# Optimization experiments

Hardware: AMD Instinct MI355X
Metric: run time of the kernel (lower is better)

The kernel has to match this reference:

```python
import jax, jax.numpy as jnp
import numpy as np

B, S, D, H = 4, 1024, 1024, 16
E = D // H  # head_dim = 64
N = 2 * H  # number of slots


def _ln(x, g, b, eps=1e-5):
    m = x.mean(-1, keepdims=True)
    v = ((x - m) ** 2).mean(-1, keepdims=True)
    return (x - m) / jnp.sqrt(v + eps) * g + b


def _feat(x):
    # F.elu(x, 1.0) + 1.0
    return jax.nn.elu(x) + 1.0


def setup_inputs() -> dict:
    key = jax.random.key(0)
    ks = jax.random.split(key, 40)
    w = lambda k, shape: jax.random.normal(k, shape, jnp.float32) * 0.02
    z = lambda shape: jnp.zeros(shape, jnp.float32)
    o = lambda shape: jnp.ones(shape, jnp.float32)
    return {
        'x': jax.random.normal(ks[0], (B, S, D), jnp.float32),
        'ln1_g': o(D), 'ln1_b': z(D), 'ln2_g': o(D), 'ln2_b': z(D),
        'Wq': w(ks[1], (D, D)), 'bq': z(D),
        'Wk': w(ks[2], (D, D)), 'bk': z(D),
        'Wv': w(ks[3], (D, D)), 'bv': z(D),
        'Wf': w(ks[4], (D, D)), 'bf': z(D),
        'Wr1': w(ks[5], (D, 2 * D)), 'br1': z(2 * D),
        'Wr2': w(ks[6], (2 * D, D)), 'br2': z(D),
        'Wip': w(ks[7], (D, N * E)), 'bip': z(N * E),
        'Wtq': w(ks[8], (E, E)), 'btq': z(E),
        'Wtk': w(ks[9], (E, E)), 'btk': z(E),
        'Wtv': w(ks[10], (E, E)), 'btv': z(E),
        'lnp_g': o(E), 'lnp_b': z(E),
        'Wl1': w(ks[11], (E, 2 * E)), 'bl1': z(2 * E),
        'Wl2': w(ks[12], (2 * E, E)), 'bl2': z(E),
        'Wsp': w(ks[13], (2 * E, E)), 'bsp': z(E),
    }


def reference(x, ln1_g, ln1_b, ln2_g, ln2_b, Wq, bq, Wk, bk, Wv, bv, Wf, bf,
              Wr1, br1, Wr2, br2, Wip, bip, Wtq, btq, Wtk, btk, Wtv, btv,
              lnp_g, lnp_b, Wl1, bl1, Wl2, bl2, Wsp, bsp):
    xn = _ln(x, ln1_g, ln1_b)
    # main q/k/v
    q = (xn @ Wq + bq).reshape(B, S, H, E).transpose(0, 2, 1, 3) / np.sqrt(E)  # [B,H,S,E]
    k = (xn @ Wk + bk).reshape(B, S, H, E)
    v = (xn @ Wv + bv).reshape(B, S, H, E)
    kv0 = jnp.concatenate([k, v], axis=2)  # [B,S,2H,E] initial slots

    # --- competitive (slot) attention, 3 iterations ---
    inp = (xn @ Wip + bip).reshape(B, S, N, E)
    kk = _feat(inp @ Wtk + btk)          # [B,S,N,E]
    vv = inp @ Wtv + btv                 # [B,S,N,E]
    slots = kv0
    scale = 1.0 / E                      # slot_size = head_dim
    for _ in range(3):
        qq = (slots @ Wtq + btq) + kv0
        qq = _feat(qq * (E ** -0.5))
        logits = jnp.einsum('bswe,bsne->bswn', kk, qq)
        attn = jax.nn.softmax(logits, axis=3) + 1e-6
        attn = attn / attn.sum(axis=2, keepdims=True)
        upd = jnp.einsum('bswn,bswe->bsne', attn, vv)
        h = _ln(upd, lnp_g, lnp_b)
        h = jax.nn.relu(h @ Wl1 + bl1) @ Wl2 + bl2
        slots = slots + h * scale
    # slot_dropout is eval-mode identity
    slots = jnp.concatenate([kv0, slots], axis=-1) @ Wsp + bsp  # [B,S,2H,E]

    k2 = slots[:, :, :H].transpose(0, 2, 3, 1)  # [B,H,E,S]
    v2 = slots[:, :, H:].transpose(0, 2, 1, 3)  # [B,H,S,E]
    qf = _feat(q)
    kf = _feat(k2)
    score = qf @ kf                              # [B,H,S,S]
    score = score / (score.sum(-1, keepdims=True) + 1e-5)
    out = (score @ v2).transpose(0, 2, 1, 3).reshape(B, S, D)
    out = out @ Wf + bf
    out = x + out
    res = out
    h = _ln(out, ln2_g, ln2_b)
    h = jax.nn.relu(h @ Wr1 + br1) @ Wr2 + br2  # dropouts are eval-mode identity
    return res + h
```

## Files before the change

kernel.cpp:

```cpp
#include <hip/hip_runtime.h>
#include <hip/hip_bf16.h>

typedef __hip_bfloat16 bf16t;
typedef short short8 __attribute__((ext_vector_type(8)));
typedef short short4v __attribute__((ext_vector_type(4)));
typedef float f32x4 __attribute__((ext_vector_type(4)));


__device__ __forceinline__ float featf(float x) { return x > 0.f ? x + 1.f : __expf(x); }
__device__ __forceinline__ float featf_s(float x) { return x > 0.f ? x + 1.f : expf(x); }
__device__ __forceinline__ float frcp(float x) { return __builtin_amdgcn_rcpf(x); }
__device__ __forceinline__ float ldf(const bf16t* p, size_t i) { return __bfloat162float(p[i]); }
__device__ __forceinline__ float ldf(const float* p, size_t i) { return p[i]; }
__device__ __forceinline__ void stf(bf16t* p, size_t i, float v) { p[i] = __float2bfloat16(v); }
__device__ __forceinline__ void stf(float* p, size_t i, float v) { p[i] = v; }
__device__ __forceinline__ float b2f(unsigned short u) {
    unsigned int x = ((unsigned int)u) << 16; float f; __builtin_memcpy(&f, &x, 4); return f;
}
__device__ __forceinline__ unsigned short f2b(float f) {
    bf16t h = __float2bfloat16(f); unsigned short u; __builtin_memcpy(&u, &h, 2); return u;
}
__device__ __forceinline__ void gl_lds16(const short* g, short* l) {
    __builtin_amdgcn_global_load_lds((const __attribute__((address_space(1))) unsigned int*)g,
                                     (__attribute__((address_space(3))) unsigned int*)l, 16, 0, 0);
}
#define MFMA16(a, b, c) __builtin_amdgcn_mfma_f32_16x16x32_bf16((a), (b), (c), 0, 0, 0)

__global__ __launch_bounds__(256) void fill_k(float* __restrict__ out, int n, float v) {
    int i = blockIdx.x * 256 + threadIdx.x;
    if (i < n) out[i] = v;
}

__global__ __launch_bounds__(256) void multi_transpose_k(const float* __restrict__ s0, const float* __restrict__ s1,
                                                         const float* __restrict__ s2, const float* __restrict__ s3,
                                                         bf16t* __restrict__ d0, bf16t* __restrict__ d1,
                                                         bf16t* __restrict__ d2, bf16t* __restrict__ d3,
                                                         int R0, int C0, int R1, int C1, int R2, int C2, int R3, int C3,
                                                         int e0, int e1, int e2) {
    __shared__ bf16t tile[32][33];
    int b = blockIdx.x;
    const float* W; bf16t* Wt; int C, R, lb;
    if (b < e0)      { W = s0; Wt = d0; R = R0; C = C0; lb = b; }
    else if (b < e1) { W = s1; Wt = d1; R = R1; C = C1; lb = b - e0; }
    else if (b < e2) { W = s2; Wt = d2; R = R2; C = C2; lb = b - e1; }
    else             { W = s3; Wt = d3; R = R3; C = C3; lb = b - e2; }
    int tiles_c = C >> 5;
    int c0 = (lb % tiles_c) * 32, r0 = (lb / tiles_c) * 32;
    int tx = threadIdx.x & 31, ty = threadIdx.x >> 5;
    #pragma unroll
    for (int i = 0; i < 32; i += 8)
        tile[ty + i][tx] = __float2bfloat16(W[(size_t)(r0 + ty + i) * C + (c0 + tx)]);
    __syncthreads();
    #pragma unroll
    for (int i = 0; i < 32; i += 8)
        Wt[(size_t)(c0 + ty + i) * R + (r0 + tx)] = tile[tx][ty + i];
}

__global__ __launch_bounds__(256) void small_prep_k(const float* __restrict__ Wtk,
                                                    const float* __restrict__ Wtv,
                                                    const float* __restrict__ Wtq,
                                                    const float* __restrict__ Wl1,
                                                    const float* __restrict__ Wl2,
                                                    const float* __restrict__ Wsp,
                                                    const float* __restrict__ bk,
                                                    const float* __restrict__ bv,
                                                    const float* __restrict__ bip,
                                                    const float* __restrict__ bq,
                                                    const float* __restrict__ btk,
                                                    const float* __restrict__ btv,
                                                    bf16t* __restrict__ WtkvT,
                                                    bf16t* __restrict__ WtqI,
                                                    bf16t* __restrict__ Wl1T,
                                                    bf16t* __restrict__ Wl2T,
                                                    bf16t* __restrict__ WspT,
                                                    float* __restrict__ bcat,
                                                    float* __restrict__ bcat2) {
    int b = blockIdx.x, tid = threadIdx.x;
    if (b == 0) {
        for (int i = tid; i < 8192; i += 256) {
            int n2 = i >> 6, e = i & 63;
            float v = (n2 < 64) ? Wtk[e * 64 + n2] : Wtv[e * 64 + (n2 - 64)];
            WtkvT[i] = __float2bfloat16(v);
        }
    } else if (b == 1) {
        for (int i = tid; i < 8192; i += 256) {
            int e = i >> 7, k = i & 127;
            float v = (k < 64) ? Wtq[k * 64 + e] : ((k - 64 == e) ? 1.f : 0.f);
            WtqI[i] = __float2bfloat16(v);
        }
    } else if (b == 2) {
        for (int i = tid; i < 8192; i += 256) { int n = i >> 6, k = i & 63; Wl1T[i] = __float2bfloat16(Wl1[k * 128 + n]); }
    } else if (b == 3) {
        for (int i = tid; i < 8192; i += 256) { int n = i >> 7, k = i & 127; Wl2T[i] = __float2bfloat16(Wl2[k * 64 + n]); }
    } else if (b == 4) {
        for (int i = tid; i < 8192; i += 256) { int n = i >> 7, k = i & 127; WspT[i] = __float2bfloat16(Wsp[k * 64 + n]); }
    } else if (b == 5) {
        for (int i = tid; i < 5120; i += 256) {
            float v;
            if (i < 1024) v = bk[i];
            else if (i < 2048) v = bv[i - 1024];
            else if (i < 4096) v = bip[i - 2048];
            else v = bq[i - 4096];
            bcat[i] = v;
        }
    } else {
        if (tid < 128) bcat2[tid] = (tid < 64) ? btk[tid] : btv[tid - 64];
    }
}

__global__ __launch_bounds__(256) void ln_kernel(const float* __restrict__ X,
                                                 const float* __restrict__ g,
                                                 const float* __restrict__ b,
                                                 bf16t* __restrict__ Y) {
    int t = blockIdx.x, tid = threadIdx.x;
    size_t base = (size_t)t * 1024 + tid * 4;
    float v0 = X[base + 0], v1 = X[base + 1], v2 = X[base + 2], v3 = X[base + 3];
    float s = v0 + v1 + v2 + v3;
    float q = v0 * v0 + v1 * v1 + v2 * v2 + v3 * v3;
    __shared__ float rs[4], rq[4];
    for (int o = 32; o > 0; o >>= 1) { s += __shfl_down(s, o); q += __shfl_down(q, o); }
    int wid = tid >> 6, lane = tid & 63;
    if (lane == 0) { rs[wid] = s; rq[wid] = q; }
    __syncthreads();
    float S = rs[0] + rs[1] + rs[2] + rs[3];
    float Q = rq[0] + rq[1] + rq[2] + rq[3];
    float mean = S * (1.f / 1024.f);
    float var = Q * (1.f / 1024.f) - mean * mean;
    float rstd = rsqrtf(var + 1e-5f);
    int c = tid * 4;
    stf(Y, base + 0, (v0 - mean) * rstd * g[c + 0] + b[c + 0]);
    stf(Y, base + 1, (v1 - mean) * rstd * g[c + 1] + b[c + 1]);
    stf(Y, base + 2, (v2 - mean) * rstd * g[c + 2] + b[c + 2]);
    stf(Y, base + 3, (v3 - mean) * rstd * g[c + 3] + b[c + 3]);
}

template <int MODE, typename TC, typename TADD>
__global__ __launch_bounds__(256) void gemm64_k(const bf16t* __restrict__ A,
                                                const bf16t* __restrict__ Bt,
                                                const float* __restrict__ bias,
                                                const TADD* __restrict__ add,
                                                TC* __restrict__ C,
                                                int M, int N, int K, int ldC) {
    __shared__ short As[64 * 32];
    __shared__ short Bs[128 * 32];
    int tid = threadIdx.x;
    int wave = tid >> 6, lane = tid & 63;
    int l16 = lane & 15, quad = lane >> 4;
    int tilesM = M >> 6;
    int bid = (blockIdx.x & 7) * (gridDim.x >> 3) + (blockIdx.x >> 3);
    int tm = bid % tilesM;
    int tn = bid / tilesM;

    int lrow = lane >> 2;
    int lseg = (lane & 3) * 8;
    const short* Ag = (const short*)A + (size_t)(tm * 64 + wave * 16 + lrow) * K + lseg;
    const short* Bg = (const short*)Bt + (size_t)(tn * 128 + wave * 32 + lrow) * K + lseg;
    const short* Bg2 = Bg + (size_t)16 * K;
    short* Asw = As + (wave * 16) * 32;
    short* Bsw = Bs + (wave * 32) * 32;
    short* Bsw2 = Bsw + 16 * 32;

    f32x4 acc[4][2] = {};
    for (int k0 = 0; k0 < K; k0 += 32) {
        gl_lds16(Ag + k0, Asw);
        gl_lds16(Bg + k0, Bsw);
        gl_lds16(Bg2 + k0, Bsw2);
        __syncthreads();
        short8 av[4], bv[2];
        #pragma unroll
        for (int i = 0; i < 4; i++)
            av[i] = *(const short8*)(As + (i * 16 + l16) * 32 + quad * 8);
        #pragma unroll
        for (int j = 0; j < 2; j++)
            bv[j] = *(const short8*)(Bs + (wave * 32 + j * 16 + l16) * 32 + quad * 8);
        #pragma unroll
        for (int i = 0; i < 4; i++)
            #pragma unroll
            for (int j = 0; j < 2; j++)
                acc[i][j] = MFMA16(av[i], bv[j], acc[i][j]);
        __syncthreads();
    }

    #pragma unroll
    for (int j = 0; j < 2; j++) {
        int col = tn * 128 + wave * 32 + j * 16 + l16;
        float bcol = bias[col];
        #pragma unroll
        for (int i = 0; i < 4; i++) {
            int row0 = tm * 64 + i * 16 + quad * 4;
            #pragma unroll
            for (int r = 0; r < 4; r++) {
                int row = row0 + r;
                float v = acc[i][j][r] + bcol;
                float outv;
                if constexpr (MODE == 0) outv = v;
                else if constexpr (MODE == 4) outv = fmaxf(v, 0.f);
                else if constexpr (MODE == 5) outv = v + ldf(add, (size_t)row * N + col);
                else outv = v;
                stf(C, (size_t)row * ldC + col, outv);
            }
        }
    }
}

template <int MODE, typename TC, typename TADD>
__global__ __launch_bounds__(256) void gemm6464_k(const bf16t* __restrict__ A,
                                                  const bf16t* __restrict__ Bt,
                                                  const float* __restrict__ bias,
                                                  const TADD* __restrict__ add,
                                                  TC* __restrict__ C,
                                                  int M, int N, int K, int ldC) {
    __shared__ short As[64 * 32];
    __shared__ short Bs[64 * 32];
    int tid = threadIdx.x;
    int wave = tid >> 6, lane = tid & 63;
    int l16 = lane & 15, quad = lane >> 4;
    int tilesM = M >> 6;
    int bid = (blockIdx.x & 7) * (gridDim.x >> 3) + (blockIdx.x >> 3);
    int tm = bid % tilesM;
    int tn = bid / tilesM;

    int lrow = lane >> 2;
    int lseg = (lane & 3) * 8;
    const short* Ag = (const short*)A + (size_t)(tm * 64 + wave * 16 + lrow) * K + lseg;
    const short* Bg = (const short*)Bt + (size_t)(tn * 64 + wave * 16 + lrow) * K + lseg;
    short* Asw = As + (wave * 16) * 32;
    short* Bsw = Bs + (wave * 16) * 32;

    f32x4 acc[4] = {};
    for (int k0 = 0; k0 < K; k0 += 32) {
        gl_lds16(Ag + k0, Asw);
        gl_lds16(Bg + k0, Bsw);
        __syncthreads();
        short8 av[4], bv;
        #pragma unroll
        for (int i = 0; i < 4; i++)
            av[i] = *(const short8*)(As + (i * 16 + l16) * 32 + quad * 8);
        bv = *(const short8*)(Bs + (wave * 16 + l16) * 32 + quad * 8);
        #pragma unroll
        for (int i = 0; i < 4; i++)
            acc[i] = MFMA16(av[i], bv, acc[i]);
        __syncthreads();
    }

    {
        int col = tn * 64 + wave * 16 + l16;
        float bcol = bias[col];
        #pragma unroll
        for (int i = 0; i < 4; i++) {
            int row0 = tm * 64 + i * 16 + quad * 4;
            #pragma unroll
            for (int r = 0; r < 4; r++) {
                int row = row0 + r;
                float v = acc[i][r] + bcol;
                float outv;
                if constexpr (MODE == 0) outv = v;
                else if constexpr (MODE == 4) outv = fmaxf(v, 0.f);
                else if constexpr (MODE == 5) outv = v + ldf(add, (size_t)row * N + col);
                else outv = v;
                stf(C, (size_t)row * ldC + col, outv);
            }
        }
    }
}

__global__ __launch_bounds__(256) void gemm_proj_k(const bf16t* __restrict__ A,
                                                   const bf16t* __restrict__ Bt,
                                                   const float* __restrict__ bias,
                                                   bf16t* __restrict__ kv0,
                                                   bf16t* __restrict__ inp,
                                                   bf16t* __restrict__ qf) {
    __shared__ short As[128 * 32];
    __shared__ short Bs[128 * 32];
    const int K = 1024;
    int tid = threadIdx.x;
    int wave = tid >> 6, lane = tid & 63;
    int l16 = lane & 15, quad = lane >> 4;
    int bid = (blockIdx.x & 7) * (gridDim.x >> 3) + (blockIdx.x >> 3);
    int tm = bid & 31;
    int tn = bid >> 5;
    int wm = wave >> 1, wn = wave & 1;

    int lrow = lane >> 2;
    int lseg = (lane & 3) * 8;
    const short* Ag = (const short*)A + (size_t)(tm * 128 + wave * 32 + lrow) * K + lseg;
    const short* Ag2 = Ag + (size_t)16 * K;
    const short* Bg = (const short*)Bt + (size_t)(tn * 128 + wave * 32 + lrow) * K + lseg;
    const short* Bg2 = Bg + (size_t)16 * K;
    short* Asw = As + (wave * 32) * 32;
    short* Asw2 = Asw + 16 * 32;
    short* Bsw = Bs + (wave * 32) * 32;
    short* Bsw2 = Bsw + 16 * 32;

    f32x4 acc[4][4] = {};
    for (int k0 = 0; k0 < K; k0 += 32) {
        gl_lds16(Ag + k0, Asw);
        gl_lds16(Ag2 + k0, Asw2);
        gl_lds16(Bg + k0, Bsw);
        gl_lds16(Bg2 + k0, Bsw2);
        __syncthreads();
        short8 av[4], bv[4];
        #pragma unroll
        for (int i = 0; i < 4; i++)
            av[i] = *(const short8*)(As + (wm * 64 + i * 16 + l16) * 32 + quad * 8);
        #pragma unroll
        for (int j = 0; j < 4; j++)
            bv[j] = *(const short8*)(Bs + (wn * 64 + j * 16 + l16) * 32 + quad * 8);
        #pragma unroll
        for (int i = 0; i < 4; i++)
            #pragma unroll
            for (int j = 0; j < 4; j++)
                acc[i][j] = MFMA16(av[i], bv[j], acc[i][j]);
        __syncthreads();
    }

    #pragma unroll
    for (int j = 0; j < 4; j++) {
        int col = tn * 128 + wn * 64 + j * 16 + l16;
        float bcol = bias[col];
        #pragma unroll
        for (int i = 0; i < 4; i++) {
            int row0 = tm * 128 + wm * 64 + i * 16 + quad * 4;
            #pragma unroll
            for (int r = 0; r < 4; r++) {
                int row = row0 + r;
                float v = acc[i][j][r] + bcol;
                if (tn < 16) stf(kv0, (size_t)row * 2048 + col, v);
                else if (tn < 32) stf(inp, (size_t)row * 2048 + (col - 2048), v);
                else stf(qf, (size_t)row * 1024 + (col - 4096), featf(v * 0.125f));
            }
        }
    }
}

__global__ __launch_bounds__(256) void gemm_kv_k(const bf16t* __restrict__ A,
                                                 const bf16t* __restrict__ Bt,
                                                 const float* __restrict__ bias,
                                                 bf16t* __restrict__ kkO,
                                                 bf16t* __restrict__ vvTO) {
    int wave = threadIdx.x >> 6, lane = threadIdx.x & 63;
    int tile = blockIdx.x * 4 + wave;
    int tm = tile >> 1, tn = tile & 1;
    int l16 = lane & 15, quad = lane >> 4;
    f32x4 acc[4][4] = {};
    const short* Ab = (const short*)A + (size_t)(tm * 64 + l16) * 64;
    const short* Bb = (const short*)Bt + (size_t)(tn * 64 + l16) * 64;
    #pragma unroll
    for (int k0 = 0; k0 < 64; k0 += 32) {
        int ka = k0 + quad * 8;
        short8 av[4], bv[4];
        #pragma unroll
        for (int i = 0; i < 4; i++) av[i] = *(const short8*)(Ab + (size_t)i * 16 * 64 + ka);
        #pragma unroll
        for (int j = 0; j < 4; j++) bv[j] = *(const short8*)(Bb + (size_t)j * 16 * 64 + ka);
        #pragma unroll
        for (int i = 0; i < 4; i++)
            #pragma unroll
            for (int j = 0; j < 4; j++)
                acc[i][j] = MFMA16(av[i], bv[j], acc[i][j]);
    }
    #pragma unroll
    for (int j = 0; j < 4; j++) {
        int col = j * 16 + l16;
        float bcol = bias[tn * 64 + col];
        #pragma unroll
        for (int i = 0; i < 4; i++) {
            int row0 = tm * 64 + i * 16 + quad * 4;
            #pragma unroll
            for (int r = 0; r < 4; r++) {
                int row = row0 + r;
                float v = acc[i][j][r] + bcol;
                if (tn == 0) kkO[(size_t)row * 64 + col] = __float2bfloat16(featf(v));
                else stf(vvTO, (size_t)(row >> 5) * 2048 + (size_t)col * 32 + (row & 31), v);
            }
        }
    }
}

__global__ __launch_bounds__(256) void gemm_cat_k(const bf16t* __restrict__ A1,
                                                  const bf16t* __restrict__ A2,
                                                  const bf16t* __restrict__ Bt,
                                                  const float* __restrict__ bias,
                                                  bf16t* __restrict__ C, int M) {
    int wave = threadIdx.x >> 6;
    int lane = threadIdx.x & 63;
    int tiles = M >> 6;
    int tile = blockIdx.x * 4 + wave;
    if (tile >= tiles) return;
    int tm = tile;
    int l16 = lane & 15, quad = lane >> 4;
    f32x4 acc[4][4] = {};
    #pragma unroll
    for (int p = 0; p < 2; p++) {
        const short* Ab = (const short*)(p ? A2 : A1) + (size_t)(tm * 64 + l16) * 64;
        const short* Bb = (const short*)Bt + (size_t)l16 * 128 + p * 64;
        #pragma unroll
        for (int k0 = 0; k0 < 64; k0 += 32) {
            int ka = k0 + quad * 8;
            short8 av[4], bv[4];
            #pragma unroll
            for (int i = 0; i < 4; i++) av[i] = *(const short8*)(Ab + (size_t)i * 16 * 64 + ka);
            #pragma unroll
            for (int j = 0; j < 4; j++) bv[j] = *(const short8*)(Bb + (size_t)j * 16 * 128 + ka);
            #pragma unroll
            for (int i = 0; i < 4; i++)
                #pragma unroll
                for (int j = 0; j < 4; j++)
                    acc[i][j] = MFMA16(av[i], bv[j], acc[i][j]);
        }
    }
    #pragma unroll
    for (int j = 0; j < 4; j++) {
        int col = j * 16 + l16;
        float bcol = bias[col];
        #pragma unroll
        for (int i = 0; i < 4; i++) {
            int row0 = tm * 64 + i * 16 + quad * 4;
            #pragma unroll
            for (int r = 0; r < 4; r++)
                C[(size_t)(row0 + r) * 64 + col] = __float2bfloat16(acc[i][j][r] + bcol);
        }
    }
}

__global__ __launch_bounds__(256) void slot_all_k(const bf16t* __restrict__ kv0,
                                                  const bf16t* __restrict__ kk,
                                                  const bf16t* __restrict__ vvT,
                                                  const bf16t* __restrict__ WtqI,
                                                  const float* __restrict__ btq,
                                                  const float* __restrict__ lnpg,
                                                  const float* __restrict__ lnpb,
                                                  const bf16t* __restrict__ Wl1T,
                                                  const float* __restrict__ bl1,
                                                  const bf16t* __restrict__ Wl2T,
                                                  const float* __restrict__ bl2,
                                                  bf16t* __restrict__ slots_out,
                                                  int zoff) {
    __shared__ short slotsS[4][32 * 72];
    __shared__ short scratch[4][32 * 72];
    int wave = threadIdx.x >> 6, lane = threadIdx.x & 63;
    int l16 = lane & 15, quad = lane >> 4;
    int t = blockIdx.x * 4 + wave;
    short* S = slotsS[wave];
    short* X = scratch[wave];
    size_t tbase = (size_t)t * 2048;

    {
        const short* src = (const short*)kv0 + tbase;
        #pragma unroll
        for (int p = 0; p < 4; p++) {
            int idx = p * 512 + lane * 8;
            int row = idx >> 6, col = idx & 63;
            *(short8*)(S + row * 72 + col) = *(const short8*)(src + idx);
        }
    }

    #pragma unroll 1
    for (int it = 0; it < 3; it++) {
        int vo = it * zoff;
        f32x4 aq[2][4] = {};
        #pragma unroll
        for (int k0 = 0; k0 < 4; k0++) {
            short8 af[2];
            #pragma unroll
            for (int i = 0; i < 2; i++) {
                if (k0 < 2)
                    af[i] = *(const short8*)(S + (i * 16 + l16) * 72 + k0 * 32 + quad * 8);
                else
                    af[i] = *(const short8*)((const short*)kv0 + tbase + (size_t)((i * 16 + l16) * 64 + (k0 - 2) * 32 + quad * 8 + vo));
            }
            #pragma unroll
            for (int j = 0; j < 4; j++) {
                short8 bf_ = *(const short8*)((const short*)WtqI + (size_t)((j * 16 + l16) * 128 + k0 * 32 + quad * 8 + vo));
                #pragma unroll
                for (int i = 0; i < 2; i++) aq[i][j] = MFMA16(af[i], bf_, aq[i][j]);
            }
        }
        {
            float btqv[4];
            #pragma unroll
            for (int j = 0; j < 4; j++) btqv[j] = btq[j * 16 + l16 + vo];
            #pragma unroll
            for (int i = 0; i < 2; i++)
                #pragma unroll
                for (int j = 0; j < 4; j++)
                    #pragma unroll
                    for (int r = 0; r < 4; r++) {
                        int n = i * 16 + quad * 4 + r, e = j * 16 + l16;
                        X[n * 72 + e] = (short)f2b(featf_s((aq[i][j][r] + btqv[j]) * 0.125f));
                    }
        }
        f32x4 al[2][2] = {};
        #pragma unroll
        for (int k0 = 0; k0 < 2; k0++) {
            short8 ak[2], bf_[2];
            #pragma unroll
            for (int i = 0; i < 2; i++)
                ak[i] = *(const short8*)((const short*)kk + tbase + (size_t)((i * 16 + l16) * 64 + k0 * 32 + quad * 8 + vo));
            #pragma unroll
            for (int j = 0; j < 2; j++)
                bf_[j] = *(const short8*)(X + (j * 16 + l16) * 72 + k0 * 32 + quad * 8);
            #pragma unroll
            for (int i = 0; i < 2; i++)
                #pragma unroll
                for (int j = 0; j < 2; j++)
                    al[i][j] = MFMA16(ak[i], bf_[j], al[i][j]);
        }
        #pragma unroll
        for (int i = 0; i < 2; i++)
            #pragma unroll
            for (int r = 0; r < 4; r++) {
                float m = fmaxf(al[i][0][r], al[i][1][r]);
                #pragma unroll
                for (int d = 1; d < 16; d <<= 1) m = fmaxf(m, __shfl_xor(m, d));
                float e0 = expf(al[i][0][r] - m), e1 = expf(al[i][1][r] - m);
                float s = e0 + e1;
                #pragma unroll
                for (int d = 1; d < 16; d <<= 1) s += __shfl_xor(s, d);
                float inv = 1.f / s;
                al[i][0][r] = e0 * inv + 1e-6f;
                al[i][1][r] = e1 * inv + 1e-6f;
            }
        #pragma unroll
        for (int j = 0; j < 2; j++) {
            float cs = 0.f;
            #pragma unroll
            for (int i = 0; i < 2; i++)
                #pragma unroll
                for (int r = 0; r < 4; r++) cs += al[i][j][r];
            cs += __shfl_xor(cs, 16);
            cs += __shfl_xor(cs, 32);
            float inv = 1.f / cs;
            #pragma unroll
            for (int i = 0; i < 2; i++)
                #pragma unroll
                for (int r = 0; r < 4; r++) al[i][j][r] *= inv;
        }
        #pragma unroll
        for (int i = 0; i < 2; i++)
            #pragma unroll
            for (int j = 0; j < 2; j++)
                #pragma unroll
                for (int r = 0; r < 4; r++) {
                    int w = i * 16 + quad * 4 + r, n = j * 16 + l16;
                    X[n * 40 + w] = (short)f2b(al[i][j][r]);
                }
        f32x4 au[2][4] = {};
        {
            short8 af[2];
            #pragma unroll
            for (int i = 0; i < 2; i++)
                af[i] = *(const short8*)(X + (i * 16 + l16) * 40 + quad * 8);
            #pragma unroll
            for (int j = 0; j < 4; j++) {
                short8 bf_ = *(const short8*)((const short*)vvT + tbase + (size_t)((j * 16 + l16) * 32 + quad * 8 + vo));
                #pragma unroll
                for (int i = 0; i < 2; i++) au[i][j] = MFMA16(af[i], bf_, au[i][j]);
            }
        }
        {
            float lgv[4], lbv[4];
            #pragma unroll
            for (int j = 0; j < 4; j++) { lgv[j] = lnpg[j * 16 + l16 + vo]; lbv[j] = lnpb[j * 16 + l16 + vo]; }
            #pragma unroll
            for (int i = 0; i < 2; i++)
                #pragma unroll
                for (int r = 0; r < 4; r++) {
                    float s1 = 0.f, s2 = 0.f;
                    #pragma unroll
                    for (int j = 0; j < 4; j++) { float u = au[i][j][r]; s1 += u; s2 += u * u; }
                    #pragma unroll
                    for (int d = 1; d < 16; d <<= 1) { s1 += __shfl_xor(s1, d); s2 += __shfl_xor(s2, d); }
                    float mean = s1 * (1.f / 64.f);
                    float var = s2 * (1.f / 64.f) - mean * mean;
                    float rstd = rsqrtf(var + 1e-5f);
                    int n = i * 16 + quad * 4 + r;
                    #pragma unroll
                    for (int j = 0; j < 4; j++)
                        X[n * 72 + j * 16 + l16] = (short)f2b((au[i][j][r] - mean) * rstd * lgv[j] + lbv[j]);
                }
        }
        short8 a1[2][2];
        #pragma unroll
        for (int i = 0; i < 2; i++)
            #pragma unroll
            for (int k0 = 0; k0 < 2; k0++)
                a1[i][k0] = *(const short8*)(X + (i * 16 + l16) * 72 + k0 * 32 + quad * 8);
        f32x4 ac2[2][4] = {};
        #pragma unroll
        for (int c = 0; c < 2; c++) {
            f32x4 ac1[2][4] = {};
            #pragma unroll
            for (int k0 = 0; k0 < 2; k0++)
                #pragma unroll
                for (int j = 0; j < 4; j++) {
                    short8 bf_ = *(const short8*)((const short*)Wl1T + (size_t)(((c * 4 + j) * 16 + l16) * 64 + k0 * 32 + quad * 8 + vo));
                    #pragma unroll
                    for (int i = 0; i < 2; i++) ac1[i][j] = MFMA16(a1[i][k0], bf_, ac1[i][j]);
                }
            {
                float bl1v[4];
                #pragma unroll
                for (int j = 0; j < 4; j++) bl1v[j] = bl1[(c * 4 + j) * 16 + l16 + vo];
                #pragma unroll
                for (int i = 0; i < 2; i++)
                    #pragma unroll
                    for (int j = 0; j < 4; j++)
                        #pragma unroll
                        for (int r = 0; r < 4; r++) {
                            int n = i * 16 + quad * 4 + r;
                            X[n * 72 + j * 16 + l16] = (short)f2b(fmaxf(ac1[i][j][r] + bl1v[j], 0.f));
                        }
            }
            #pragma unroll
            for (int kc = 0; kc < 2; kc++) {
                short8 a2[2];
                #pragma unroll
                for (int i = 0; i < 2; i++)
                    a2[i] = *(const short8*)(X + (i * 16 + l16) * 72 + kc * 32 + quad * 8);
                int k1 = c * 2 + kc;
                #pragma unroll
                for (int j = 0; j < 4; j++) {
                    short8 bf_ = *(const short8*)((const short*)Wl2T + (size_t)((j * 16 + l16) * 128 + k1 * 32 + quad * 8 + vo));
                    #pragma unroll
                    for (int i = 0; i < 2; i++) ac2[i][j] = MFMA16(a2[i], bf_, ac2[i][j]);
                }
            }
        }
        {
            float bl2v[4];
            #pragma unroll
            for (int j = 0; j < 4; j++) bl2v[j] = bl2[j * 16 + l16 + vo];
            #pragma unroll
            for (int i = 0; i < 2; i++)
                #pragma unroll
                for (int j = 0; j < 4; j++)
                    #pragma unroll
                    for (int r = 0; r < 4; r++) {
                        int n = i * 16 + quad * 4 + r, e = j * 16 + l16;
                        float old = b2f((unsigned short)S[n * 72 + e]);
                        S[n * 72 + e] = (short)f2b(old + (ac2[i][j][r] + bl2v[j]) * (1.f / 64.f));
                    }
        }
    }
    {
        short* dst = (short*)slots_out + tbase;
        #pragma unroll
        for (int p = 0; p < 4; p++) {
            int idx = p * 512 + lane * 8;
            int row = idx >> 6, col = idx & 63;
            *(short8*)(dst + idx) = *(const short8*)(S + row * 72 + col);
        }
    }
}

__global__ __launch_bounds__(256) void kv_outer_k(const bf16t* __restrict__ slotsO,
                                                  float* __restrict__ Kpart,
                                                  float* __restrict__ kspart) {
    __shared__ short kfT[64 * 72];
    __shared__ short v2T[64 * 72];
    __shared__ float ksred[8][64];
    int blk = blockIdx.x;
    int bh = blk >> 2, chunk = blk & 3;
    int b = bh >> 4, h = bh & 15;
    int tid = threadIdx.x;
    int wave = tid >> 6, lane = tid & 63;
    int l16 = lane & 15, quad = lane >> 4;
    int m0 = wave * 16;

    int sgrp = tid >> 5;
    int e0 = (tid & 31) * 2;
    float ks0 = 0.f, ks1 = 0.f;
    f32x4 acc[4];
    #pragma unroll
    for (int j = 0; j < 4; j++) acc[j] = (f32x4){0.f, 0.f, 0.f, 0.f};

    for (int tile = chunk * 4; tile < chunk * 4 + 4; tile++) {
        #pragma unroll
        for (int p = 0; p < 8; p++) {
            int sl = p * 8 + sgrp;
            size_t row = ((size_t)(b * 1024 + tile * 64 + sl)) * 2048;
            unsigned int dk = *(const unsigned int*)((const unsigned short*)slotsO + row + h * 64 + e0);
            float f0 = featf(b2f((unsigned short)(dk & 0xffff)));
            float f1 = featf(b2f((unsigned short)(dk >> 16)));
            ks0 += f0; ks1 += f1;
            kfT[e0 * 72 + sl] = (short)f2b(f0);
            kfT[(e0 + 1) * 72 + sl] = (short)f2b(f1);
            unsigned int dv = *(const unsigned int*)((const unsigned short*)slotsO + row + (16 + h) * 64 + e0);
            v2T[e0 * 72 + sl] = (short)(dv & 0xffff);
            v2T[(e0 + 1) * 72 + sl] = (short)(dv >> 16);
        }
        __syncthreads();
        #pragma unroll
        for (int k2 = 0; k2 < 2; k2++) {
            short8 a = *(const short8*)(v2T + (m0 + l16) * 72 + k2 * 32 + quad * 8);
            #pragma unroll
            for (int j = 0; j < 4; j++) {
                short8 bv = *(const short8*)(kfT + (j * 16 + l16) * 72 + k2 * 32 + quad * 8);
                acc[j] = MFMA16(a, bv, acc[j]);
            }
        }
        __syncthreads();
    }

    float* Km = Kpart + (size_t)blk * 4096;
    #pragma unroll
    for (int j = 0; j < 4; j++)
        #pragma unroll
        for (int r = 0; r < 4; r++)
            Km[(m0 + quad * 4 + r) * 64 + j * 16 + l16] = acc[j][r];

    ksred[sgrp][e0] = ks0;
    ksred[sgrp][e0 + 1] = ks1;
    __syncthreads();
    if (tid < 64) {
        float s = 0.f;
        #pragma unroll
        for (int r = 0; r < 8; r++) s += ksred[r][tid];
        kspart[blk * 64 + tid] = s;
    }
}

__global__ __launch_bounds__(256) void kred_k(const float* __restrict__ Kpart,
                                              const float* __restrict__ kspart,
                                              bf16t* __restrict__ KmatT,
                                              float* __restrict__ ksum) {
    int gid = blockIdx.x * 256 + threadIdx.x;
    int idx = gid * 4;
    int bh = idx >> 12, j = idx & 4095;
    const float* p = Kpart + (size_t)(bh * 4) * 4096 + j;
    f32x4 a = *(const f32x4*)p;
    f32x4 bq = *(const f32x4*)(p + 4096);
    f32x4 c = *(const f32x4*)(p + 8192);
    f32x4 d = *(const f32x4*)(p + 12288);
    f32x4 r = a + bq + c + d;
    short4v o;
    #pragma unroll
    for (int k = 0; k < 4; k++) o[k] = (short)f2b(r[k]);
    *(short4v*)((short*)KmatT + idx) = o;
    if (gid < 4096) {
        int bh2 = gid >> 6, e = gid & 63;
        const float* q = kspart + (size_t)(bh2 * 4) * 64 + e;
        ksum[gid] = q[0] + q[64] + q[128] + q[192];
    }
}

__global__ __launch_bounds__(256) void attn_gemm_k(const bf16t* __restrict__ qf,
                                                   const bf16t* __restrict__ KmatT,
                                                   const float* __restrict__ ksum,
                                                   bf16t* __restrict__ out) {
    __shared__ float dls[4][64];
    int wave = threadIdx.x >> 6, lane = threadIdx.x & 63;
    int wt = blockIdx.x * 4 + wave;
    int bh = wt >> 4, st = wt & 15;
    int b = bh >> 4, h = bh & 15;
    int l16 = lane & 15, quad = lane >> 4;
    int s0 = st * 64;
    {
        const unsigned short* qr = (const unsigned short*)qf + (size_t)(b * 1024 + s0 + lane) * 1024 + h * 64;
        const float* ks = ksum + (size_t)bh * 64;
        float d = 0.f;
        #pragma unroll
        for (int e = 0; e < 64; e++) d += b2f(qr[e]) * ks[e];
        dls[wave][lane] = frcp(d + 1e-5f);
    }
    const short* Aq = (const short*)qf + (size_t)(b * 1024 + s0 + l16) * 1024 + h * 64;
    const short* Bk = (const short*)KmatT + (size_t)bh * 4096;
    f32x4 acc[4][4] = {};
    #pragma unroll
    for (int k0 = 0; k0 < 64; k0 += 32) {
        int ka = k0 + quad * 8;
        short8 av[4], bv[4];
        #pragma unroll
        for (int i = 0; i < 4; i++) av[i] = *(const short8*)(Aq + (size_t)i * 16 * 1024 + ka);
        #pragma unroll
        for (int j = 0; j < 4; j++) bv[j] = *(const short8*)(Bk + (j * 16 + l16) * 64 + ka);
        #pragma unroll
        for (int i = 0; i < 4; i++)
            #pragma unroll
            for (int j = 0; j < 4; j++)
                acc[i][j] = MFMA16(av[i], bv[j], acc[i][j]);
    }
    #pragma unroll
    for (int i = 0; i < 4; i++) {
        #pragma unroll
        for (int r = 0; r < 4; r++) {
            int trow = i * 16 + quad * 4 + r;
            int t = b * 1024 + s0 + trow;
            float di = dls[wave][trow];
            size_t ob = (size_t)t * 1024 + h * 64;
            #pragma unroll
            for (int j = 0; j < 4; j++)
                out[ob + j * 16 + l16] = __float2bfloat16(acc[i][j][r] * di);
        }
    }
}

#define LAUNCH_GEMM64(MODE, TCT, TADDT, A_, Bt_, bias_, add_, C_, M_, N_, K_, ldC_)          \
    do {                                                                                     \
        int tiles__ = ((M_) >> 6) * ((N_) >> 7);                                             \
        gemm64_k<MODE, TCT, TADDT><<<tiles__, 256, 0, stream>>>(                             \
            (const bf16t*)(A_), (const bf16t*)(Bt_), (const float*)(bias_),                  \
            (const TADDT*)(add_), (TCT*)(C_), (M_), (N_), (K_), (ldC_));                     \
    } while (0)

#define LAUNCH_GEMM6464(MODE, TCT, TADDT, A_, Bt_, bias_, add_, C_, M_, N_, K_, ldC_)        \
    do {                                                                                     \
        int tiles__ = ((M_) >> 6) * ((N_) >> 6);                                             \
        gemm6464_k<MODE, TCT, TADDT><<<tiles__, 256, 0, stream>>>(                           \
            (const bf16t*)(A_), (const bf16t*)(Bt_), (const float*)(bias_),                  \
            (const TADDT*)(add_), (TCT*)(C_), (M_), (N_), (K_), (ldC_));                     \
    } while (0)

extern "C" void kernel_launch(void* const* d_in, const int* in_sizes, int n_in,
                              void* d_out, int out_size, void* d_ws, size_t ws_size,
                              hipStream_t stream) {
    (void)in_sizes; (void)n_in;
    const float* x    = (const float*)d_in[0];
    const float* ln1g = (const float*)d_in[1];
    const float* ln1b = (const float*)d_in[2];
    const float* ln2g = (const float*)d_in[3];
    const float* ln2b = (const float*)d_in[4];
    const float* Wq  = (const float*)d_in[5];  const float* bq  = (const float*)d_in[6];
    const float* Wk  = (const float*)d_in[7];  const float* bk  = (const float*)d_in[8];
    const float* Wv  = (const float*)d_in[9];  const float* bv  = (const float*)d_in[10];
    const float* Wf  = (const float*)d_in[11]; const float* bWf = (const float*)d_in[12];
    const float* Wr1 = (const float*)d_in[13]; const float* br1 = (const float*)d_in[14];
    const float* Wr2 = (const float*)d_in[15]; const float* br2 = (const float*)d_in[16];
    const float* Wip = (const float*)d_in[17]; const float* bip = (const float*)d_in[18];
    const float* Wtq = (const float*)d_in[19]; const float* btq = (const float*)d_in[20];
    const float* Wtk = (const float*)d_in[21]; const float* btk = (const float*)d_in[22];
    const float* Wtv = (const float*)d_in[23]; const float* btv = (const float*)d_in[24];
    const float* lnpg= (const float*)d_in[25]; const float* lnpb= (const float*)d_in[26];
    const float* Wl1 = (const float*)d_in[27]; const float* bl1 = (const float*)d_in[28];
    const float* Wl2 = (const float*)d_in[29]; const float* bl2 = (const float*)d_in[30];
    const float* Wsp = (const float*)d_in[31]; const float* bsp = (const float*)d_in[32];

    char* ws = (char*)d_ws;
    size_t off = 0;
    auto alloc = [&](size_t bytes) -> char* {
        off = (off + 255) & ~(size_t)255;
        char* p = ws + off;
        off += bytes;
        return p;
    };
    const size_t T = 4096, TS = 131072;
    const size_t MB8 = T * 1024 * 2, MB16 = T * 2048 * 2;
    bf16t* R_xn   = (bf16t*)alloc(MB8);
    bf16t* R_h1   = (bf16t*)alloc(MB8);
    bf16t* R_kv0  = (bf16t*)alloc(MB16);
    bf16t* R_inp  = (bf16t*)alloc(MB16);
    bf16t* R_kk   = (bf16t*)alloc(MB16);
    bf16t* R_vv   = (bf16t*)alloc(MB16);
    bf16t* R_sl   = (bf16t*)alloc(MB16);
    bf16t* Wcat   = (bf16t*)alloc(5120 * 1024 * 2);
    bf16t* WtkvT = (bf16t*)alloc(128 * 64 * 2);
    bf16t* WtqI = (bf16t*)alloc(64 * 128 * 2);
    bf16t* Wl1T = (bf16t*)alloc(128 * 64 * 2);
    bf16t* Wl2T = (bf16t*)alloc(64 * 128 * 2);
    bf16t* WspT = (bf16t*)alloc(64 * 128 * 2);
    float* bcat = (float*)alloc(5120 * 4);
    float* bcat2 = (float*)alloc(128 * 4);
    bf16t* KmatT = (bf16t*)alloc(64 * 4096 * 2);
    float* ksum = (float*)alloc(64 * 64 * 4);
    float* Kpart = (float*)alloc(256 * 4096 * 4);
    float* kspart = (float*)alloc(256 * 64 * 4);

    if (off > ws_size) {
        fill_k<<<(out_size + 255) / 256, 256, 0, stream>>>((float*)d_out, out_size, 1000.f);
        return;
    }
    float* R_res = (float*)R_vv;
    bf16t* WfT  = R_kv0;
    bf16t* Wr1T = R_kv0 + (size_t)1024 * 1024;
    bf16t* Wr2T = R_kv0 + (size_t)3072 * 1024;

    small_prep_k<<<7, 256, 0, stream>>>(Wtk, Wtv, Wtq, Wl1, Wl2, Wsp, bk, bv, bip, bq, btk, btv,
                                        WtkvT, WtqI, Wl1T, Wl2T, WspT, bcat, bcat2);

    ln_kernel<<<4096, 256, 0, stream>>>(x, ln1g, ln1b, R_xn);

    multi_transpose_k<<<5120, 256, 0, stream>>>(
        Wk, Wv, Wip, Wq,
        Wcat, Wcat + (size_t)1024 * 1024, Wcat + (size_t)2048 * 1024, Wcat + (size_t)4096 * 1024,
        1024, 1024, 1024, 1024, 1024, 2048, 1024, 1024,
        1024, 2048, 4096);

    gemm_proj_k<<<1280, 256, 0, stream>>>(R_xn, Wcat, bcat, R_kv0, R_inp, R_h1);

    gemm_kv_k<<<1024, 256, 0, stream>>>(R_inp, WtkvT, bcat2, R_kk, R_vv);

    slot_all_k<<<1024, 256, 0, stream>>>(R_kv0, R_kk, R_vv, WtqI, btq, lnpg, lnpb,
                                         Wl1T, bl1, Wl2T, bl2, R_sl, 0);

    gemm_cat_k<<<512, 256, 0, stream>>>(R_kv0, R_sl, WspT, bsp, R_kk, 131072);

    multi_transpose_k<<<5120, 256, 0, stream>>>(
        Wf, Wr1, Wr2, Wr2,
        WfT, Wr1T, Wr2T, Wr2T,
        1024, 1024, 1024, 2048, 2048, 1024, 2048, 1024,
        1024, 3072, 5120);

    kv_outer_k<<<256, 256, 0, stream>>>(R_kk, Kpart, kspart);
    kred_k<<<256, 256, 0, stream>>>(Kpart, kspart, KmatT, ksum);

    attn_gemm_k<<<256, 256, 0, stream>>>(R_h1, KmatT, ksum, R_inp);

    LAUNCH_GEMM6464(5, float, float, R_inp, WfT, bWf, x, R_res, 4096, 1024, 1024, 1024);

    ln_kernel<<<4096, 256, 0, stream>>>(R_res, ln2g, ln2b, R_xn);
    LAUNCH_GEMM64(4, bf16t, bf16t, R_xn, Wr1T, br1, nullptr, R_sl, 4096, 2048, 1024, 2048);
    LAUNCH_GEMM6464(5, float, float, R_sl, Wr2T, br2, R_res, (float*)d_out, 4096, 1024, 2048, 1024);
}
```

Before: 507.6 us.

## Fuse prep kernels into stage1 and tail, deepen GEMM K-tile to 64

Merges small weight prep, first layernorm and the weight transposes into one launch, and folds the tail weight transposes into the kv outer-product kernel, cutting kernel launches and letting independent work share the GPU. The gemm64 and gemm6464 kernels now stage K=64 per iteration instead of 32, which halves the number of barriers per GEMM in exchange for double the LDS use. Mixed-role kernels raise shared memory per block to the maximum of all roles, which may lower occupancy for the lighter branches.

```diff
diff --git a/kernel.cpp b/kernel.cpp
--- a/kernel.cpp
+++ b/kernel.cpp
@@ -31,19 +31,8 @@
     if (i < n) out[i] = v;
 }
 
-__global__ __launch_bounds__(256) void multi_transpose_k(const float* __restrict__ s0, const float* __restrict__ s1,
-                                                         const float* __restrict__ s2, const float* __restrict__ s3,
-                                                         bf16t* __restrict__ d0, bf16t* __restrict__ d1,
-                                                         bf16t* __restrict__ d2, bf16t* __restrict__ d3,
-                                                         int R0, int C0, int R1, int C1, int R2, int C2, int R3, int C3,
-                                                         int e0, int e1, int e2) {
-    __shared__ bf16t tile[32][33];
-    int b = blockIdx.x;
-    const float* W; bf16t* Wt; int C, R, lb;
-    if (b < e0)      { W = s0; Wt = d0; R = R0; C = C0; lb = b; }
-    else if (b < e1) { W = s1; Wt = d1; R = R1; C = C1; lb = b - e0; }
-    else if (b < e2) { W = s2; Wt = d2; R = R2; C = C2; lb = b - e1; }
-    else             { W = s3; Wt = d3; R = R3; C = C3; lb = b - e2; }
+__device__ __forceinline__ void dev_transpose32(bf16t (*tile)[33], const float* W, bf16t* Wt,
+                                                int R, int C, int lb) {
     int tiles_c = C >> 5;
     int c0 = (lb % tiles_c) * 32, r0 = (lb / tiles_c) * 32;
     int tx = threadIdx.x & 31, ty = threadIdx.x >> 5;
@@ -56,68 +45,14 @@
         Wt[(size_t)(c0 + ty + i) * R + (r0 + tx)] = tile[tx][ty + i];
 }
 
-__global__ __launch_bounds__(256) void small_prep_k(const float* __restrict__ Wtk,
-                                                    const float* __restrict__ Wtv,
-                                                    const float* __restrict__ Wtq,
-                                                    const float* __restrict__ Wl1,
-                                                    const float* __restrict__ Wl2,
-                                                    const float* __restrict__ Wsp,
-                                                    const float* __restrict__ bk,
-                                                    const float* __restrict__ bv,
-                                                    const float* __restrict__ bip,
-                                                    const float* __restrict__ bq,
-                                                    const float* __restrict__ btk,
-                                                    const float* __restrict__ btv,
-                                                    bf16t* __restrict__ WtkvT,
-                                                    bf16t* __restrict__ WtqI,
-                                                    bf16t* __restrict__ Wl1T,
-                                                    bf16t* __restrict__ Wl2T,
-                                                    bf16t* __restrict__ WspT,
-                                                    float* __restrict__ bcat,
-                                                    float* __restrict__ bcat2) {
-    int b = blockIdx.x, tid = threadIdx.x;
-    if (b == 0) {
-        for (int i = tid; i < 8192; i += 256) {
-            int n2 = i >> 6, e = i & 63;
-            float v = (n2 < 64) ? Wtk[e * 64 + n2] : Wtv[e * 64 + (n2 - 64)];
-            WtkvT[i] = __float2bfloat16(v);
-        }
-    } else if (b == 1) {
-        for (int i = tid; i < 8192; i += 256) {
-            int e = i >> 7, k = i & 127;
-            float v = (k < 64) ? Wtq[k * 64 + e] : ((k - 64 == e) ? 1.f : 0.f);
-            WtqI[i] = __float2bfloat16(v);
-        }
-    } else if (b == 2) {
-        for (int i = tid; i < 8192; i += 256) { int n = i >> 6, k = i & 63; Wl1T[i] = __float2bfloat16(Wl1[k * 128 + n]); }
-    } else if (b == 3) {
-        for (int i = tid; i < 8192; i += 256) { int n = i >> 7, k = i & 127; Wl2T[i] = __float2bfloat16(Wl2[k * 64 + n]); }
-    } else if (b == 4) {
-        for (int i = tid; i < 8192; i += 256) { int n = i >> 7, k = i & 127; WspT[i] = __float2bfloat16(Wsp[k * 64 + n]); }
-    } else if (b == 5) {
-        for (int i = tid; i < 5120; i += 256) {
-            float v;
-            if (i < 1024) v = bk[i];
-            else if (i < 2048) v = bv[i - 1024];
-            else if (i < 4096) v = bip[i - 2048];
-            else v = bq[i - 4096];
-            bcat[i] = v;
-        }
-    } else {
-        if (tid < 128) bcat2[tid] = (tid < 64) ? btk[tid] : btv[tid - 64];
-    }
-}
-
-__global__ __launch_bounds__(256) void ln_kernel(const float* __restrict__ X,
-                                                 const float* __restrict__ g,
-                                                 const float* __restrict__ b,
-                                                 bf16t* __restrict__ Y) {
-    int t = blockIdx.x, tid = threadIdx.x;
+__device__ __forceinline__ void dev_ln(float* rs, float* rq,
+                                       const float* X, const float* g, const float* b,
+                                       bf16t* Y, int t) {
+    int tid = threadIdx.x;
     size_t base = (size_t)t * 1024 + tid * 4;
     float v0 = X[base + 0], v1 = X[base + 1], v2 = X[base + 2], v3 = X[base + 3];
     float s = v0 + v1 + v2 + v3;
     float q = v0 * v0 + v1 * v1 + v2 * v2 + v3 * v3;
-    __shared__ float rs[4], rq[4];
     for (int o = 32; o > 0; o >>= 1) { s += __shfl_down(s, o); q += __shfl_down(q, o); }
     int wid = tid >> 6, lane = tid & 63;
     if (lane == 0) { rs[wid] = s; rq[wid] = q; }
@@ -134,6 +69,89 @@
     stf(Y, base + 3, (v3 - mean) * rstd * g[c + 3] + b[c + 3]);
 }
 
+__global__ __launch_bounds__(256) void ln_kernel(const float* __restrict__ X,
+                                                 const float* __restrict__ g,
+                                                 const float* __restrict__ b,
+                                                 bf16t* __restrict__ Y) {
+    __shared__ float rs[4], rq[4];
+    dev_ln(rs, rq, X, g, b, Y, blockIdx.x);
+}
+
+__global__ __launch_bounds__(256) void stage1_k(const float* __restrict__ x,
+                                                const float* __restrict__ ln1g,
+                                                const float* __restrict__ ln1b,
+                                                bf16t* __restrict__ xn,
+                                                const float* __restrict__ Wk,
+                                                const float* __restrict__ Wv,
+                                                const float* __restrict__ Wip,
+                                                const float* __restrict__ Wq,
+                                                bf16t* __restrict__ Wcat,
+                                                const float* __restrict__ Wtk,
+                                                const float* __restrict__ Wtv,
+                                                const float* __restrict__ Wtq,
+                                                const float* __restrict__ Wl1,
+                                                const float* __restrict__ Wl2,
+                                                const float* __restrict__ Wsp,
+                                                const float* __restrict__ bk,
+                                                const float* __restrict__ bv,
+                                                const float* __restrict__ bip,
+                                                const float* __restrict__ bq,
+                                                const float* __restrict__ btk,
+                                                const float* __restrict__ btv,
+                                                bf16t* __restrict__ WtkvT,
+                                                bf16t* __restrict__ WtqI,
+                                                bf16t* __restrict__ Wl1T,
+                                                bf16t* __restrict__ Wl2T,
+                                                bf16t* __restrict__ WspT,
+                                                float* __restrict__ bcat,
+                                                float* __restrict__ bcat2) {
+    __shared__ bf16t tile[32][33];
+    __shared__ float rs[4], rq[4];
+    int b = blockIdx.x, tid = threadIdx.x;
+    if (b < 5120) {
+        const float* W; bf16t* Wt; int R, C, lb;
+        if (b < 1024)      { W = Wk;  Wt = Wcat;                          R = 1024; C = 1024; lb = b; }
+        else if (b < 2048) { W = Wv;  Wt = Wcat + (size_t)1024 * 1024;    R = 1024; C = 1024; lb = b - 1024; }
+        else if (b < 4096) { W = Wip; Wt = Wcat + (size_t)2048 * 1024;    R = 1024; C = 2048; lb = b - 2048; }
+        else               { W = Wq;  Wt = Wcat + (size_t)4096 * 1024;    R = 1024; C = 1024; lb = b - 4096; }
+        dev_transpose32(tile, W, Wt, R, C, lb);
+    } else if (b < 9216) {
+        dev_ln(rs, rq, x, ln1g, ln1b, xn, b - 5120);
+    } else {
+        int pb = b - 9216;
+        if (pb == 0) {
+            for (int i = tid; i < 8192; i += 256) {
+                int n2 = i >> 6, e = i & 63;
+                float v = (n2 < 64) ? Wtk[e * 64 + n2] : Wtv[e * 64 + (n2 - 64)];
+                WtkvT[i] = __float2bfloat16(v);
+            }
+        } else if (pb == 1) {
+            for (int i = tid; i < 8192; i += 256) {
+                int e = i >> 7, k = i & 127;
+                float v = (k < 64) ? Wtq[k * 64 + e] : ((k - 64 == e) ? 1.f : 0.f);
+                WtqI[i] = __float2bfloat16(v);
+            }
+        } else if (pb == 2) {
+            for (int i = tid; i < 8192; i += 256) { int n = i >> 6, k = i & 63; Wl1T[i] = __float2bfloat16(Wl1[k * 128 + n]); }
+        } else if (pb == 3) {
+            for (int i = tid; i < 8192; i += 256) { int n = i >> 7, k = i & 127; Wl2T[i] = __float2bfloat16(Wl2[k * 64 + n]); }
+        } else if (pb == 4) {
+            for (int i = tid; i < 8192; i += 256) { int n = i >> 7, k = i & 127; WspT[i] = __float2bfloat16(Wsp[k * 64 + n]); }
+        } else if (pb == 5) {
+            for (int i = tid; i < 5120; i += 256) {
+                float v;
+                if (i < 1024) v = bk[i];
+                else if (i < 2048) v = bv[i - 1024];
+                else if (i < 4096) v = bip[i - 2048];
+                else v = bq[i - 4096];
+                bcat[i] = v;
+            }
+        } else {
+            if (tid < 128) bcat2[tid] = (tid < 64) ? btk[tid] : btv[tid - 64];
+        }
+    }
+}
+
 template <int MODE, typename TC, typename TADD>
 __global__ __launch_bounds__(256) void gemm64_k(const bf16t* __restrict__ A,
                                                 const bf16t* __restrict__ Bt,
@@ -141,8 +159,8 @@
                                                 const TADD* __restrict__ add,
                                                 TC* __restrict__ C,
                                                 int M, int N, int K, int ldC) {
-    __shared__ short As[64 * 32];
-    __shared__ short Bs[128 * 32];
+    __shared__ short As[64 * 64];
+    __shared__ short Bs[128 * 64];
     int tid = threadIdx.x;
     int wave = tid >> 6, lane = tid & 63;
     int l16 = lane & 15, quad = lane >> 4;
@@ -151,33 +169,45 @@
     int tm = bid % tilesM;
     int tn = bid / tilesM;
 
-    int lrow = lane >> 2;
-    int lseg = (lane & 3) * 8;
-    const short* Ag = (const short*)A + (size_t)(tm * 64 + wave * 16 + lrow) * K + lseg;
-    const short* Bg = (const short*)Bt + (size_t)(tn * 128 + wave * 32 + lrow) * K + lseg;
-    const short* Bg2 = Bg + (size_t)16 * K;
-    short* Asw = As + (wave * 16) * 32;
-    short* Bsw = Bs + (wave * 32) * 32;
-    short* Bsw2 = Bsw + 16 * 32;
+    int lrow8 = lane >> 3;
+    int lseg8 = (lane & 7) * 8;
+    const short* Ag  = (const short*)A + (size_t)(tm * 64 + wave * 16 + lrow8) * K + lseg8;
+    const short* Ag2 = Ag + (size_t)8 * K;
+    const short* Bg  = (const short*)Bt + (size_t)(tn * 128 + wave * 32 + lrow8) * K + lseg8;
+    const short* Bg2 = Bg + (size_t)8 * K;
+    const short* Bg3 = Bg + (size_t)16 * K;
+    const short* Bg4 = Bg + (size_t)24 * K;
+    short* Asw  = As + (wave * 16) * 64;
+    short* Asw2 = Asw + 8 * 64;
+    short* Bsw  = Bs + (wave * 32) * 64;
+    short* Bsw2 = Bsw + 8 * 64;
+    short* Bsw3 = Bsw + 16 * 64;
+    short* Bsw4 = Bsw + 24 * 64;
 
     f32x4 acc[4][2] = {};
-    for (int k0 = 0; k0 < K; k0 += 32) {
+    for (int k0 = 0; k0 < K; k0 += 64) {
         gl_lds16(Ag + k0, Asw);
+        gl_lds16(Ag2 + k0, Asw2);
         gl_lds16(Bg + k0, Bsw);
         gl_lds16(Bg2 + k0, Bsw2);
+        gl_lds16(Bg3 + k0, Bsw3);
+        gl_lds16(Bg4 + k0, Bsw4);
         __syncthreads();
-        short8 av[4], bv[2];
-        #pragma unroll
-        for (int i = 0; i < 4; i++)
-            av[i] = *(const short8*)(As + (i * 16 + l16) * 32 + quad * 8);
-        #pragma unroll
-        for (int j = 0; j < 2; j++)
-            bv[j] = *(const short8*)(Bs + (wave * 32 + j * 16 + l16) * 32 + quad * 8);
-        #pragma unroll
-        for (int i = 0; i < 4; i++)
+        #pragma unroll
+        for (int kk = 0; kk < 2; kk++) {
+            short8 av[4], bv[2];
+            #pragma unroll
+            for (int i = 0; i < 4; i++)
+                av[i] = *(const short8*)(As + (i * 16 + l16) * 64 + kk * 32 + quad * 8);
             #pragma unroll
             for (int j = 0; j < 2; j++)
-                acc[i][j] = MFMA16(av[i], bv[j], acc[i][j]);
+                bv[j] = *(const short8*)(Bs + (wave * 32 + j * 16 + l16) * 64 + kk * 32 + quad * 8);
+            #pragma unroll
+            for (int i = 0; i < 4; i++)
+                #pragma unroll
+                for (int j = 0; j < 2; j++)
+                    acc[i][j] = MFMA16(av[i], bv[j], acc[i][j]);
+        }
         __syncthreads();
     }
 
@@ -210,8 +240,8 @@
                                                   const TADD* __restrict__ add,
                                                   TC* __restrict__ C,
                                                   int M, int N, int K, int ldC) {
-    __shared__ short As[64 * 32];
-    __shared__ short Bs[64 * 32];
+    __shared__ short As[64 * 64];
+    __shared__ short Bs[64 * 64];
     int tid = threadIdx.x;
     int wave = tid >> 6, lane = tid & 63;
     int l16 = lane & 15, quad = lane >> 4;
@@ -220,26 +250,35 @@
     int tm = bid % tilesM;
     int tn = bid / tilesM;
 
-    int lrow = lane >> 2;
-    int lseg = (lane & 3) * 8;
-    const short* Ag = (const short*)A + (size_t)(tm * 64 + wave * 16 + lrow) * K + lseg;
-    const short* Bg = (const short*)Bt + (size_t)(tn * 64 + wave * 16 + lrow) * K + lseg;
-    short* Asw = As + (wave * 16) * 32;
-    short* Bsw = Bs + (wave * 16) * 32;
+    int lrow8 = lane >> 3;
+    int lseg8 = (lane & 7) * 8;
+    const short* Ag  = (const short*)A + (size_t)(tm * 64 + wave * 16 + lrow8) * K + lseg8;
+    const short* Ag2 = Ag + (size_t)8 * K;
+    const short* Bg  = (const short*)Bt + (size_t)(tn * 64 + wave * 16 + lrow8) * K + lseg8;
+    const short* Bg2 = Bg + (size_t)8 * K;
+    short* Asw  = As + (wave * 16) * 64;
+    short* Asw2 = Asw + 8 * 64;
+    short* Bsw  = Bs + (wave * 16) * 64;
+    short* Bsw2 = Bsw + 8 * 64;
 
     f32x4 acc[4] = {};
-    for (int k0 = 0; k0 < K; k0 += 32) {
+    for (int k0 = 0; k0 < K; k0 += 64) {
         gl_lds16(Ag + k0, Asw);
+        gl_lds16(Ag2 + k0, Asw2);
         gl_lds16(Bg + k0, Bsw);
+        gl_lds16(Bg2 + k0, Bsw2);
         __syncthreads();
-        short8 av[4], bv;
-        #pragma unroll
-        for (int i = 0; i < 4; i++)
-            av[i] = *(const short8*)(As + (i * 16 + l16) * 32 + quad * 8);
-        bv = *(const short8*)(Bs + (wave * 16 + l16) * 32 + quad * 8);
-        #pragma unroll
-        for (int i = 0; i < 4; i++)
-            acc[i] = MFMA16(av[i], bv, acc[i]);
+        #pragma unroll
+        for (int kk = 0; kk < 2; kk++) {
+            short8 av[4], bv;
+            #pragma unroll
+            for (int i = 0; i < 4; i++)
+                av[i] = *(const short8*)(As + (i * 16 + l16) * 64 + kk * 32 + quad * 8);
+            bv = *(const short8*)(Bs + (wave * 16 + l16) * 64 + kk * 32 + quad * 8);
+            #pragma unroll
+            for (int i = 0; i < 4; i++)
+                acc[i] = MFMA16(av[i], bv, acc[i]);
+        }
         __syncthreads();
     }
 
@@ -654,13 +693,30 @@
     }
 }
 
-__global__ __launch_bounds__(256) void kv_outer_k(const bf16t* __restrict__ slotsO,
+__global__ __launch_bounds__(256) void tail_mix_k(const bf16t* __restrict__ slotsO,
                                                   float* __restrict__ Kpart,
-                                                  float* __restrict__ kspart) {
+                                                  float* __restrict__ kspart,
+                                                  const float* __restrict__ Wf,
+                                                  const float* __restrict__ Wr1,
+                                                  const float* __restrict__ Wr2,
+                                                  bf16t* __restrict__ WfT,
+                                                  bf16t* __restrict__ Wr1T,
+                                                  bf16t* __restrict__ Wr2T) {
     __shared__ short kfT[64 * 72];
     __shared__ short v2T[64 * 72];
     __shared__ float ksred[8][64];
-    int blk = blockIdx.x;
+    __shared__ bf16t tile[32][33];
+    int gb = blockIdx.x;
+    if (gb >= 256) {
+        int lb = gb - 256;
+        const float* W; bf16t* Wt; int R, C;
+        if (lb < 1024)      { W = Wf;  Wt = WfT;  R = 1024; C = 1024; }
+        else if (lb < 3072) { W = Wr1; Wt = Wr1T; R = 1024; C = 2048; lb -= 1024; }
+        else                { W = Wr2; Wt = Wr2T; R = 2048; C = 1024; lb -= 3072; }
+        dev_transpose32(tile, W, Wt, R, C, lb);
+        return;
+    }
+    int blk = gb;
     int bh = blk >> 2, chunk = blk & 3;
     int b = bh >> 4, h = bh & 15;
     int tid = threadIdx.x;
@@ -675,11 +731,11 @@
     #pragma unroll
     for (int j = 0; j < 4; j++) acc[j] = (f32x4){0.f, 0.f, 0.f, 0.f};
 
-    for (int tile = chunk * 4; tile < chunk * 4 + 4; tile++) {
+    for (int tile2 = chunk * 4; tile2 < chunk * 4 + 4; tile2++) {
         #pragma unroll
         for (int p = 0; p < 8; p++) {
             int sl = p * 8 + sgrp;
-            size_t row = ((size_t)(b * 1024 + tile * 64 + sl)) * 2048;
+            size_t row = ((size_t)(b * 1024 + tile2 * 64 + sl)) * 2048;
             unsigned int dk = *(const unsigned int*)((const unsigned short*)slotsO + row + h * 64 + e0);
             float f0 = featf(b2f((unsigned short)(dk & 0xffff)));
             float f1 = featf(b2f((unsigned short)(dk >> 16)));
@@ -875,16 +931,11 @@
     bf16t* Wr1T = R_kv0 + (size_t)1024 * 1024;
     bf16t* Wr2T = R_kv0 + (size_t)3072 * 1024;
 
-    small_prep_k<<<7, 256, 0, stream>>>(Wtk, Wtv, Wtq, Wl1, Wl2, Wsp, bk, bv, bip, bq, btk, btv,
-                                        WtkvT, WtqI, Wl1T, Wl2T, WspT, bcat, bcat2);
-
-    ln_kernel<<<4096, 256, 0, stream>>>(x, ln1g, ln1b, R_xn);
-
-    multi_transpose_k<<<5120, 256, 0, stream>>>(
-        Wk, Wv, Wip, Wq,
-        Wcat, Wcat + (size_t)1024 * 1024, Wcat + (size_t)2048 * 1024, Wcat + (size_t)4096 * 1024,
-        1024, 1024, 1024, 1024, 1024, 2048, 1024, 1024,
-        1024, 2048, 4096);
+    stage1_k<<<9223, 256, 0, stream>>>(x, ln1g, ln1b, R_xn,
+                                       Wk, Wv, Wip, Wq, Wcat,
+                                       Wtk, Wtv, Wtq, Wl1, Wl2, Wsp,
+                                       bk, bv, bip, bq, btk, btv,
+                                       WtkvT, WtqI, Wl1T, Wl2T, WspT, bcat, bcat2);
 
     gemm_proj_k<<<1280, 256, 0, stream>>>(R_xn, Wcat, bcat, R_kv0, R_inp, R_h1);
 
@@ -895,13 +946,8 @@
 
     gemm_cat_k<<<512, 256, 0, stream>>>(R_kv0, R_sl, WspT, bsp, R_kk, 131072);
 
-    multi_transpose_k<<<5120, 256, 0, stream>>>(
-        Wf, Wr1, Wr2, Wr2,
-        WfT, Wr1T, Wr2T, Wr2T,
-        1024, 1024, 1024, 2048, 2048, 1024, 2048, 1024,
-        1024, 3072, 5120);
-
-    kv_outer_k<<<256, 256, 0, stream>>>(R_kk, Kpart, kspart);
+    tail_mix_k<<<5376, 256, 0, stream>>>(R_kk, Kpart, kspart, Wf, Wr1, Wr2, WfT, Wr1T, Wr2T);
+
     kred_k<<<256, 256, 0, stream>>>(Kpart, kspart, KmatT, ksum);
 
     attn_gemm_k<<<256, 256, 0, stream>>>(R_h1, KmatT, ksum, R_inp);
```

After: 512.5 us. No clear change (+1.0%).
